# Kernel tuning notes

Measured on AMD Instinct MI355X. Metric: run time of the kernel, lower is better.

## Reference

```python
import jax, jax.numpy as jnp
import numpy as np

CH = 256
DQK = CH // 8


def setup_inputs() -> dict:
    key = jax.random.key(0)
    ks = jax.random.split(key, 8)
    B, C, H, W = 4, CH, 64, 64
    x = jax.random.normal(ks[0], (B, C, H, W), dtype=jnp.float32)
    s = 1.0 / np.sqrt(C)
    Wq = jax.random.normal(ks[1], (DQK, C), dtype=jnp.float32) * s
    bq = jnp.zeros((DQK,), dtype=jnp.float32)
    Wk = jax.random.normal(ks[2], (DQK, C), dtype=jnp.float32) * s
    bk = jnp.zeros((DQK,), dtype=jnp.float32)
    Wv = jax.random.normal(ks[3], (C, C), dtype=jnp.float32) * s
    bv = jnp.zeros((C,), dtype=jnp.float32)
    gamma = jnp.zeros((1,), dtype=jnp.float32)
    return {"x": x, "Wq": Wq, "bq": bq, "Wk": Wk, "bk": bk, "Wv": Wv, "bv": bv, "gamma": gamma}


def reference(x, Wq, bq, Wk, bk, Wv, bv, gamma):
    B, C, H, W = x.shape
    N = H * W
    xf = x.reshape(B, C, N)                                   # [B, C, N]
    # 1x1 convs == per-position linear maps over channels
    q = jnp.einsum('dc,bcn->bdn', Wq, xf) + bq[None, :, None]  # [B, D, N]
    k = jnp.einsum('dc,bcn->bdn', Wk, xf) + bk[None, :, None]  # [B, D, N]
    v = jnp.einsum('oc,bcn->bon', Wv, xf) + bv[None, :, None]  # [B, C, N]
    # energy[b,i,j] = <q[:, i], k[:, j]>  (no 1/sqrt(d) scaling, as in source)
    energy = jnp.einsum('bdi,bdj->bij', q, k)                  # [B, N, N]
    attn = jax.nn.softmax(energy, axis=-1)                     # softmax over j
    # out[b,c,i] = sum_j v[b,c,j] * attn[b,i,j]
    out = jnp.einsum('bcj,bij->bci', v, attn)                  # [B, C, N]
    return x + gamma[0] * out.reshape(B, C, H, W)
```

## Files before the change

### kernel.cpp

```cpp
#include <hip/hip_runtime.h>
#include <hip/hip_bf16.h>

#define NB   4
#define NC   256
#define NPOS 4096
#define NDQK 32

typedef __bf16 bf16x8  __attribute__((ext_vector_type(8)));
typedef float  f32x16  __attribute__((ext_vector_type(16)));

typedef __attribute__((address_space(3))) char*       lds_ptr_t;
typedef const __attribute__((address_space(1))) char* glb_ptr_t;


__global__ __launch_bounds__(256) void proj_kernel(
    const float* __restrict__ x,
    const float* __restrict__ Wq, const float* __restrict__ bq,
    const float* __restrict__ Wk, const float* __restrict__ bk,
    const float* __restrict__ Wv, const float* __restrict__ bv,
    __hip_bfloat16* __restrict__ Qb, __hip_bfloat16* __restrict__ Kb,
    __hip_bfloat16* __restrict__ Vb)
{
    const int t   = threadIdx.x;
    const int l   = t & 63;
    const int w   = t >> 6;
    const int hi  = l >> 5;
    const int col = l & 31;
    const int row = l & 31;

    const int item = blockIdx.x * 4 + w;
    const int th   = item & 1;
    const int nch  = (item >> 1) & 63;
    const int rest = item >> 7;
    const int g    = rest % 5;
    const int b    = rest / 5;

    const float *W0, *W1, *bs0, *bs1;
    int o0 = 0, o1 = 0;
    if (g < 4) {
        o0 = g * 64; o1 = g * 64 + 32;
        W0 = Wv + (size_t)o0 * NC; W1 = Wv + (size_t)o1 * NC;
        bs0 = bv + o0; bs1 = bv + o1;
    } else {
        W0 = Wq; W1 = Wk; bs0 = bq; bs1 = bk;
    }

    bf16x8 wf0[16], wf1[16];
    const float* Wr0 = W0 + (size_t)row * NC + 8 * hi;
    const float* Wr1 = W1 + (size_t)row * NC + 8 * hi;
    #pragma unroll
    for (int kk = 0; kk < 16; ++kk) {
        float4 a0 = *reinterpret_cast<const float4*>(Wr0 + kk * 16);
        float4 c0 = *reinterpret_cast<const float4*>(Wr0 + kk * 16 + 4);
        float4 a1 = *reinterpret_cast<const float4*>(Wr1 + kk * 16);
        float4 c1 = *reinterpret_cast<const float4*>(Wr1 + kk * 16 + 4);
        bf16x8 f0, f1;
        f0[0] = (__bf16)a0.x; f0[1] = (__bf16)a0.y; f0[2] = (__bf16)a0.z; f0[3] = (__bf16)a0.w;
        f0[4] = (__bf16)c0.x; f0[5] = (__bf16)c0.y; f0[6] = (__bf16)c0.z; f0[7] = (__bf16)c0.w;
        f1[0] = (__bf16)a1.x; f1[1] = (__bf16)a1.y; f1[2] = (__bf16)a1.z; f1[3] = (__bf16)a1.w;
        f1[4] = (__bf16)c1.x; f1[5] = (__bf16)c1.y; f1[6] = (__bf16)c1.z; f1[7] = (__bf16)c1.w;
        wf0[kk] = f0; wf1[kk] = f1;
    }

    const int n0 = nch * 64 + th * 32;
    f32x16 acc0, acc1;
    #pragma unroll
    for (int r = 0; r < 16; ++r) { acc0[r] = 0.f; acc1[r] = 0.f; }

    const float* xcol = x + (size_t)b * NC * NPOS + n0 + col;
    #pragma unroll
    for (int kk = 0; kk < 16; ++kk) {
        bf16x8 bf;
        #pragma unroll
        for (int i = 0; i < 8; ++i)
            bf[i] = (__bf16)xcol[(size_t)(kk * 16 + 8 * hi + i) * NPOS];
        acc0 = __builtin_amdgcn_mfma_f32_32x32x16_bf16(wf0[kk], bf, acc0, 0, 0, 0);
        acc1 = __builtin_amdgcn_mfma_f32_32x32x16_bf16(wf1[kk], bf, acc1, 0, 0, 0);
    }

    if (g < 4) {
        __hip_bfloat16* vt = Vb + (size_t)b * NC * NPOS
                                + (size_t)(n0 >> 5) * 8192 + (size_t)g * 2048
                                + ((col >> 4) << 9) + (((col >> 3) & 1) << 8)
                                + (col & 7);
        #pragma unroll
        for (int r = 0; r < 16; ++r) {
            const int orow = (r & 3) + 8 * (r >> 2) + 4 * hi;
            vt[orow * 8]        = __float2bfloat16(acc0[r] + bs0[orow]);
            vt[1024 + orow * 8] = __float2bfloat16(acc1[r] + bs1[orow]);
        }
    } else {
        #pragma unroll
        for (int r = 0; r < 16; ++r) {
            const int orow = (r & 3) + 8 * (r >> 2) + 4 * hi;
            Qb[((size_t)(b * NPOS) + n0 + col) * NDQK + orow] =
                __float2bfloat16((acc0[r] + bs0[orow]) * 1.44269504088896f);
        }
        const int prow = (col & 0x13) | ((col & 4) << 1) | ((col & 8) >> 1);
        __hip_bfloat16* kt = Kb + (size_t)b * (NPOS * 32)
                                + (size_t)(n0 >> 5) * 1024 + prow * 8;
        #pragma unroll
        for (int r = 0; r < 16; ++r) {
            const int orow = (r & 3) + 8 * (r >> 2) + 4 * hi;
            kt[(orow >> 4) * 512 + ((orow >> 3) & 1) * 256 + (orow & 7)] =
                __float2bfloat16(acc1[r] + bs1[orow]);
        }
    }
}

__global__ __launch_bounds__(256, 1) void attn_kernel(
    const __hip_bfloat16* __restrict__ Qb,
    const __hip_bfloat16* __restrict__ Kb,
    const __hip_bfloat16* __restrict__ Vb,
    const float* __restrict__ x,
    const float* __restrict__ gamma,
    float* __restrict__ out)
{
    __shared__ __align__(16) char smem[8192 + 32768 + 16384 + 1024];
    const int t  = threadIdx.x;
    const int l  = t & 63;
    const int w  = t >> 6;
    const int hi = l >> 5;
    const int q  = l & 31;
    const int bx = blockIdx.x;
    const int b  = (bx >> 1) & 3;
    const int qt = ((bx >> 3) << 1) | (bx & 1);
    const int q0 = qt * 64;
    const int c0 = w * 64;

    const __bf16* Qp = reinterpret_cast<const __bf16*>(Qb) + (size_t)b * NPOS * NDQK;
    const __bf16* Kp = reinterpret_cast<const __bf16*>(Kb) + (size_t)b * (NPOS * 32);
    const __bf16* Vp = reinterpret_cast<const __bf16*>(Vb) + (size_t)b * NC * NPOS;

    const bf16x8 qf00 = *reinterpret_cast<const bf16x8*>(Qp + (size_t)(q0 + q) * NDQK + 8 * hi);
    const bf16x8 qf01 = *reinterpret_cast<const bf16x8*>(Qp + (size_t)(q0 + q) * NDQK + 16 + 8 * hi);
    const bf16x8 qf10 = *reinterpret_cast<const bf16x8*>(Qp + (size_t)(q0 + 32 + q) * NDQK + 8 * hi);
    const bf16x8 qf11 = *reinterpret_cast<const bf16x8*>(Qp + (size_t)(q0 + 32 + q) * NDQK + 16 + 8 * hi);
    asm volatile("" :: "v"(qf00), "v"(qf01), "v"(qf10), "v"(qf11));

    char* kb_lds = smem + w * 2048;
    char* vb_lds = smem + 8192 + w * 8192;
    __bf16* kbuf = reinterpret_cast<__bf16*>(kb_lds);
    __bf16* vbuf = reinterpret_cast<__bf16*>(vb_lds);
    __bf16* plds = reinterpret_cast<__bf16*>(smem + 40960);
    float*  lsum = reinterpret_cast<float*>(smem + 57344);

    const __bf16* ksrc = Kp + (size_t)w * 1024 + l * 8;
    const __bf16* vsrc = Vp + (size_t)w * 2048 + l * 8;

    #define DMA16(dst, src) __builtin_amdgcn_global_load_lds( \
        (glb_ptr_t)(const char*)(src), (lds_ptr_t)(dst), 16, 0, 0)
    #define DMAK(tp) do { DMA16(kb_lds, (tp)); DMA16(kb_lds + 1024, (tp) + 512); } while (0)
    #define DMAV(bi, tp) do {                                   \
        DMA16(vb_lds + (bi) * 4096,        (tp));               \
        DMA16(vb_lds + (bi) * 4096 + 1024, (tp) + 512);         \
        DMA16(vb_lds + (bi) * 4096 + 2048, (tp) + 1024);        \
        DMA16(vb_lds + (bi) * 4096 + 3072, (tp) + 1536);        \
    } while (0)

    f32x16 acc00, acc01, acc10, acc11;
    #pragma unroll
    for (int r = 0; r < 16; ++r) { acc00[r] = 0.f; acc01[r] = 0.f; acc10[r] = 0.f; acc11[r] = 0.f; }
    float lp0 = 0.f, lp1 = 0.f;

    f32x16 z16;
    #pragma unroll
    for (int r = 0; r < 16; ++r) z16[r] = 0.f;

    auto PV = [&](int tt, const __bf16* vf) {
        const bf16x8 vc0 = *reinterpret_cast<const bf16x8*>(vf);
        const bf16x8 vc1 = *reinterpret_cast<const bf16x8*>(vf + 512);
        const bf16x8 vc2 = *reinterpret_cast<const bf16x8*>(vf + 1024);
        const bf16x8 vc3 = *reinterpret_cast<const bf16x8*>(vf + 1536);
        const __bf16* pf = plds + tt * 2048 + l * 8;
        const bf16x8 pa00 = *reinterpret_cast<const bf16x8*>(pf);
        const bf16x8 pa01 = *reinterpret_cast<const bf16x8*>(pf + 512);
        const bf16x8 pa10 = *reinterpret_cast<const bf16x8*>(pf + 1024);
        const bf16x8 pa11 = *reinterpret_cast<const bf16x8*>(pf + 1536);
        acc00 = __builtin_amdgcn_mfma_f32_32x32x16_bf16(vc0, pa00, acc00, 0, 0, 0);
        acc00 = __builtin_amdgcn_mfma_f32_32x32x16_bf16(vc1, pa01, acc00, 0, 0, 0);
        acc01 = __builtin_amdgcn_mfma_f32_32x32x16_bf16(vc2, pa00, acc01, 0, 0, 0);
        acc01 = __builtin_amdgcn_mfma_f32_32x32x16_bf16(vc3, pa01, acc01, 0, 0, 0);
        acc10 = __builtin_amdgcn_mfma_f32_32x32x16_bf16(vc0, pa10, acc10, 0, 0, 0);
        acc10 = __builtin_amdgcn_mfma_f32_32x32x16_bf16(vc1, pa11, acc10, 0, 0, 0);
        acc11 = __builtin_amdgcn_mfma_f32_32x32x16_bf16(vc2, pa10, acc11, 0, 0, 0);
        acc11 = __builtin_amdgcn_mfma_f32_32x32x16_bf16(vc3, pa11, acc11, 0, 0, 0);
    };

    DMAK(ksrc);
    DMAV(0, vsrc);

    #pragma unroll 1
    for (int r = 0; r < 32; ++r) {
        asm volatile("s_waitcnt vmcnt(4)" ::: "memory");
        __builtin_amdgcn_sched_barrier(0);
        {
            const bf16x8 kc0 = *reinterpret_cast<const bf16x8*>(kbuf + l * 8);
            const bf16x8 kc1 = *reinterpret_cast<const bf16x8*>(kbuf + 512 + l * 8);
            f32x16 s0 = __builtin_amdgcn_mfma_f32_32x32x16_bf16(kc0, qf00, z16, 0, 0, 0);
            s0 = __builtin_amdgcn_mfma_f32_32x32x16_bf16(kc1, qf01, s0, 0, 0, 0);
            f32x16 s1 = __builtin_amdgcn_mfma_f32_32x32x16_bf16(kc0, qf10, z16, 0, 0, 0);
            s1 = __builtin_amdgcn_mfma_f32_32x32x16_bf16(kc1, qf11, s1, 0, 0, 0);

            float p0[16], p1[16];
            #pragma unroll
            for (int i = 0; i < 16; ++i) p0[i] = __builtin_amdgcn_exp2f(s0[i]);
            #pragma unroll
            for (int i = 0; i < 16; ++i) p1[i] = __builtin_amdgcn_exp2f(s1[i]);

            lp0 += (((p0[0] + p0[1]) + (p0[2] + p0[3])) + ((p0[4] + p0[5]) + (p0[6] + p0[7])))
                 + (((p0[8] + p0[9]) + (p0[10] + p0[11])) + ((p0[12] + p0[13]) + (p0[14] + p0[15])));
            lp1 += (((p1[0] + p1[1]) + (p1[2] + p1[3])) + ((p1[4] + p1[5]) + (p1[6] + p1[7])))
                 + (((p1[8] + p1[9]) + (p1[10] + p1[11])) + ((p1[12] + p1[13]) + (p1[14] + p1[15])));

            bf16x8 pa00, pa01, pa10, pa11;
            #pragma unroll
            for (int i = 0; i < 8; ++i) {
                pa00[i] = (__bf16)p0[i]; pa01[i] = (__bf16)p0[8 + i];
                pa10[i] = (__bf16)p1[i]; pa11[i] = (__bf16)p1[8 + i];
            }
            __bf16* pw = plds + w * 2048 + l * 8;
            *reinterpret_cast<bf16x8*>(pw)        = pa00;
            *reinterpret_cast<bf16x8*>(pw + 512)  = pa01;
            *reinterpret_cast<bf16x8*>(pw + 1024) = pa10;
            *reinterpret_cast<bf16x8*>(pw + 1536) = pa11;
        }
        asm volatile("s_waitcnt lgkmcnt(0)" ::: "memory");
        __builtin_amdgcn_s_barrier();
        __builtin_amdgcn_sched_barrier(0);

        DMAV(1, vsrc + 1 * 8192);
        asm volatile("s_waitcnt vmcnt(4)" ::: "memory");
        __builtin_amdgcn_sched_barrier(0);
        PV(0, vbuf + l * 8);

        asm volatile("s_waitcnt lgkmcnt(0)" ::: "memory");
        __builtin_amdgcn_sched_barrier(0);
        DMAV(0, vsrc + 2 * 8192);
        asm volatile("s_waitcnt vmcnt(4)" ::: "memory");
        __builtin_amdgcn_sched_barrier(0);
        PV(1, vbuf + 2048 + l * 8);

        asm volatile("s_waitcnt lgkmcnt(0)" ::: "memory");
        __builtin_amdgcn_sched_barrier(0);
        DMAV(1, vsrc + 3 * 8192);
        asm volatile("s_waitcnt vmcnt(4)" ::: "memory");
        __builtin_amdgcn_sched_barrier(0);
        PV(2, vbuf + l * 8);

        asm volatile("s_waitcnt lgkmcnt(0)" ::: "memory");
        __builtin_amdgcn_sched_barrier(0);
        ksrc += 4096;
        vsrc += 4 * 8192;
        if (r < 31) {
            DMAK(ksrc);
            DMAV(0, vsrc);
            asm volatile("s_waitcnt vmcnt(6)" ::: "memory");
        } else {
            asm volatile("s_waitcnt vmcnt(0)" ::: "memory");
        }
        __builtin_amdgcn_sched_barrier(0);
        PV(3, vbuf + 2048 + l * 8);

        asm volatile("s_waitcnt lgkmcnt(0)" ::: "memory");
        __builtin_amdgcn_s_barrier();
        __builtin_amdgcn_sched_barrier(0);
    }
    #undef DMA16
    #undef DMAK
    #undef DMAV

    const float lt0 = lp0 + __shfl_xor(lp0, 32);
    const float lt1 = lp1 + __shfl_xor(lp1, 32);
    lsum[w * 64 + 32 * hi + q] = hi ? lt1 : lt0;
    __syncthreads();

    const float gm  = gamma[0];
    const float gl0 = gm / (lsum[q]      + lsum[64 + q]  + lsum[128 + q] + lsum[192 + q]);
    const float gl1 = gm / (lsum[32 + q] + lsum[96 + q]  + lsum[160 + q] + lsum[224 + q]);
    #pragma unroll
    for (int r = 0; r < 16; ++r) {
        const int crow = (r & 3) + 8 * (r >> 2) + 4 * hi;
        const size_t g00 = ((size_t)(b * NC + c0 + crow)) * NPOS + q0 + q;
        const size_t g01 = g00 + (size_t)32 * NPOS;
        out[g00]      = x[g00]      + gl0 * acc00[r];
        out[g01]      = x[g01]      + gl0 * acc01[r];
        out[g00 + 32] = x[g00 + 32] + gl1 * acc10[r];
        out[g01 + 32] = x[g01 + 32] + gl1 * acc11[r];
    }
}

extern "C" void kernel_launch(void* const* d_in, const int* in_sizes, int n_in,
                              void* d_out, int out_size, void* d_ws, size_t ws_size,
                              hipStream_t stream) {
    (void)in_sizes; (void)n_in; (void)out_size; (void)ws_size;
    const float* x     = (const float*)d_in[0];
    const float* Wq    = (const float*)d_in[1];
    const float* bq    = (const float*)d_in[2];
    const float* Wk    = (const float*)d_in[3];
    const float* bk    = (const float*)d_in[4];
    const float* Wv    = (const float*)d_in[5];
    const float* bv    = (const float*)d_in[6];
    const float* gamma = (const float*)d_in[7];
    float* out = (float*)d_out;

    char* ws = (char*)d_ws;
    __hip_bfloat16* Qb = (__hip_bfloat16*)(ws);
    __hip_bfloat16* Kb = (__hip_bfloat16*)(ws + (1u << 20));
    __hip_bfloat16* Vb = (__hip_bfloat16*)(ws + (2u << 20));

    proj_kernel<<<640, 256, 0, stream>>>(x, Wq, bq, Wk, bk, Wv, bv, Qb, Kb, Vb);
    attn_kernel<<<256, 256, 0, stream>>>(Qb, Kb, Vb, x, gamma, out);
}
```

Measured before the change: 91.97 us.

## Deepen V prefetch pipeline to four LDS buffers per wave

Enlarges each wave's V staging area from two to four 4 KB LDS buffers and prefetches a full iteration's worth of V tiles ahead. Each PV step now waits only for its own tile and immediately refills that slot with the next iteration's tile, so global loads overlap more compute. The last iteration is peeled to drain the queue. LDS use grows to about 90 KB per block, which is fine at one block per CU but adds memory pressure and makes the hand-set vmcnt accounting more fragile.

```diff
diff --git a/kernel.cpp b/kernel.cpp
--- a/kernel.cpp
+++ b/kernel.cpp
@@ -116,7 +116,7 @@
     const float* __restrict__ gamma,
     float* __restrict__ out)
 {
-    __shared__ __align__(16) char smem[8192 + 32768 + 16384 + 1024];
+    __shared__ __align__(16) char smem[65536 + 8192 + 16384 + 1024];
     const int t  = threadIdx.x;
     const int l  = t & 63;
     const int w  = t >> 6;
@@ -138,12 +138,12 @@
     const bf16x8 qf11 = *reinterpret_cast<const bf16x8*>(Qp + (size_t)(q0 + 32 + q) * NDQK + 16 + 8 * hi);
     asm volatile("" :: "v"(qf00), "v"(qf01), "v"(qf10), "v"(qf11));
 
-    char* kb_lds = smem + w * 2048;
-    char* vb_lds = smem + 8192 + w * 8192;
-    __bf16* kbuf = reinterpret_cast<__bf16*>(kb_lds);
-    __bf16* vbuf = reinterpret_cast<__bf16*>(vb_lds);
-    __bf16* plds = reinterpret_cast<__bf16*>(smem + 40960);
-    float*  lsum = reinterpret_cast<float*>(smem + 57344);
+    char*   vb_lds = smem + w * 16384;
+    char*   kb_lds = smem + 65536 + w * 2048;
+    __bf16* vbuf   = reinterpret_cast<__bf16*>(vb_lds);
+    __bf16* kbuf   = reinterpret_cast<__bf16*>(kb_lds);
+    __bf16* plds   = reinterpret_cast<__bf16*>(smem + 73728);
+    float*  lsum   = reinterpret_cast<float*>(smem + 90112);
 
     const __bf16* ksrc = Kp + (size_t)w * 1024 + l * 8;
     const __bf16* vsrc = Vp + (size_t)w * 2048 + l * 8;
@@ -151,7 +151,7 @@
     #define DMA16(dst, src) __builtin_amdgcn_global_load_lds( \
         (glb_ptr_t)(const char*)(src), (lds_ptr_t)(dst), 16, 0, 0)
     #define DMAK(tp) do { DMA16(kb_lds, (tp)); DMA16(kb_lds + 1024, (tp) + 512); } while (0)
-    #define DMAV(bi, tp) do {                                   \
+    #define DMAV1(bi, tp) do {                                  \
         DMA16(vb_lds + (bi) * 4096,        (tp));               \
         DMA16(vb_lds + (bi) * 4096 + 1024, (tp) + 512);         \
         DMA16(vb_lds + (bi) * 4096 + 2048, (tp) + 1024);        \
@@ -167,7 +167,40 @@
     #pragma unroll
     for (int r = 0; r < 16; ++r) z16[r] = 0.f;
 
-    auto PV = [&](int tt, const __bf16* vf) {
+    auto QK = [&]() {
+        const bf16x8 kc0 = *reinterpret_cast<const bf16x8*>(kbuf + l * 8);
+        const bf16x8 kc1 = *reinterpret_cast<const bf16x8*>(kbuf + 512 + l * 8);
+        f32x16 s0 = __builtin_amdgcn_mfma_f32_32x32x16_bf16(kc0, qf00, z16, 0, 0, 0);
+        s0 = __builtin_amdgcn_mfma_f32_32x32x16_bf16(kc1, qf01, s0, 0, 0, 0);
+        f32x16 s1 = __builtin_amdgcn_mfma_f32_32x32x16_bf16(kc0, qf10, z16, 0, 0, 0);
+        s1 = __builtin_amdgcn_mfma_f32_32x32x16_bf16(kc1, qf11, s1, 0, 0, 0);
+
+        float p0[16], p1[16];
+        #pragma unroll
+        for (int i = 0; i < 16; ++i) p0[i] = __builtin_amdgcn_exp2f(s0[i]);
+        #pragma unroll
+        for (int i = 0; i < 16; ++i) p1[i] = __builtin_amdgcn_exp2f(s1[i]);
+
+        lp0 += (((p0[0] + p0[1]) + (p0[2] + p0[3])) + ((p0[4] + p0[5]) + (p0[6] + p0[7])))
+             + (((p0[8] + p0[9]) + (p0[10] + p0[11])) + ((p0[12] + p0[13]) + (p0[14] + p0[15])));
+        lp1 += (((p1[0] + p1[1]) + (p1[2] + p1[3])) + ((p1[4] + p1[5]) + (p1[6] + p1[7])))
+             + (((p1[8] + p1[9]) + (p1[10] + p1[11])) + ((p1[12] + p1[13]) + (p1[14] + p1[15])));
+
+        bf16x8 pa00, pa01, pa10, pa11;
+        #pragma unroll
+        for (int i = 0; i < 8; ++i) {
+            pa00[i] = (__bf16)p0[i]; pa01[i] = (__bf16)p0[8 + i];
+            pa10[i] = (__bf16)p1[i]; pa11[i] = (__bf16)p1[8 + i];
+        }
+        __bf16* pw = plds + w * 2048 + l * 8;
+        *reinterpret_cast<bf16x8*>(pw)        = pa00;
+        *reinterpret_cast<bf16x8*>(pw + 512)  = pa01;
+        *reinterpret_cast<bf16x8*>(pw + 1024) = pa10;
+        *reinterpret_cast<bf16x8*>(pw + 1536) = pa11;
+    };
+
+    auto PV = [&](int tt) {
+        const __bf16* vf = vbuf + tt * 2048 + l * 8;
         const bf16x8 vc0 = *reinterpret_cast<const bf16x8*>(vf);
         const bf16x8 vc1 = *reinterpret_cast<const bf16x8*>(vf + 512);
         const bf16x8 vc2 = *reinterpret_cast<const bf16x8*>(vf + 1024);
@@ -187,88 +220,51 @@
         acc11 = __builtin_amdgcn_mfma_f32_32x32x16_bf16(vc3, pa11, acc11, 0, 0, 0);
     };
 
+    #define WAIT(n) do { asm volatile("s_waitcnt vmcnt(" #n ")" ::: "memory"); \
+                         __builtin_amdgcn_sched_barrier(0); } while (0)
+    #define FENCE()  __builtin_amdgcn_sched_barrier(0)
+    #define MIDBAR() do { asm volatile("s_waitcnt lgkmcnt(0)" ::: "memory"); \
+                          __builtin_amdgcn_s_barrier(); FENCE(); } while (0)
+
     DMAK(ksrc);
-    DMAV(0, vsrc);
+    DMAV1(0, vsrc);
+    DMAV1(1, vsrc + 8192);
+    DMAV1(2, vsrc + 2 * 8192);
+    DMAV1(3, vsrc + 3 * 8192);
 
     #pragma unroll 1
-    for (int r = 0; r < 32; ++r) {
-        asm volatile("s_waitcnt vmcnt(4)" ::: "memory");
-        __builtin_amdgcn_sched_barrier(0);
-        {
-            const bf16x8 kc0 = *reinterpret_cast<const bf16x8*>(kbuf + l * 8);
-            const bf16x8 kc1 = *reinterpret_cast<const bf16x8*>(kbuf + 512 + l * 8);
-            f32x16 s0 = __builtin_amdgcn_mfma_f32_32x32x16_bf16(kc0, qf00, z16, 0, 0, 0);
-            s0 = __builtin_amdgcn_mfma_f32_32x32x16_bf16(kc1, qf01, s0, 0, 0, 0);
-            f32x16 s1 = __builtin_amdgcn_mfma_f32_32x32x16_bf16(kc0, qf10, z16, 0, 0, 0);
-            s1 = __builtin_amdgcn_mfma_f32_32x32x16_bf16(kc1, qf11, s1, 0, 0, 0);
-
-            float p0[16], p1[16];
-            #pragma unroll
-            for (int i = 0; i < 16; ++i) p0[i] = __builtin_amdgcn_exp2f(s0[i]);
-            #pragma unroll
-            for (int i = 0; i < 16; ++i) p1[i] = __builtin_amdgcn_exp2f(s1[i]);
-
-            lp0 += (((p0[0] + p0[1]) + (p0[2] + p0[3])) + ((p0[4] + p0[5]) + (p0[6] + p0[7])))
-                 + (((p0[8] + p0[9]) + (p0[10] + p0[11])) + ((p0[12] + p0[13]) + (p0[14] + p0[15])));
-            lp1 += (((p1[0] + p1[1]) + (p1[2] + p1[3])) + ((p1[4] + p1[5]) + (p1[6] + p1[7])))
-                 + (((p1[8] + p1[9]) + (p1[10] + p1[11])) + ((p1[12] + p1[13]) + (p1[14] + p1[15])));
-
-            bf16x8 pa00, pa01, pa10, pa11;
-            #pragma unroll
-            for (int i = 0; i < 8; ++i) {
-                pa00[i] = (__bf16)p0[i]; pa01[i] = (__bf16)p0[8 + i];
-                pa10[i] = (__bf16)p1[i]; pa11[i] = (__bf16)p1[8 + i];
-            }
-            __bf16* pw = plds + w * 2048 + l * 8;
-            *reinterpret_cast<bf16x8*>(pw)        = pa00;
-            *reinterpret_cast<bf16x8*>(pw + 512)  = pa01;
-            *reinterpret_cast<bf16x8*>(pw + 1024) = pa10;
-            *reinterpret_cast<bf16x8*>(pw + 1536) = pa11;
-        }
-        asm volatile("s_waitcnt lgkmcnt(0)" ::: "memory");
-        __builtin_amdgcn_s_barrier();
-        __builtin_amdgcn_sched_barrier(0);
-
-        DMAV(1, vsrc + 1 * 8192);
-        asm volatile("s_waitcnt vmcnt(4)" ::: "memory");
-        __builtin_amdgcn_sched_barrier(0);
-        PV(0, vbuf + l * 8);
-
-        asm volatile("s_waitcnt lgkmcnt(0)" ::: "memory");
-        __builtin_amdgcn_sched_barrier(0);
-        DMAV(0, vsrc + 2 * 8192);
-        asm volatile("s_waitcnt vmcnt(4)" ::: "memory");
-        __builtin_amdgcn_sched_barrier(0);
-        PV(1, vbuf + 2048 + l * 8);
-
-        asm volatile("s_waitcnt lgkmcnt(0)" ::: "memory");
-        __builtin_amdgcn_sched_barrier(0);
-        DMAV(1, vsrc + 3 * 8192);
-        asm volatile("s_waitcnt vmcnt(4)" ::: "memory");
-        __builtin_amdgcn_sched_barrier(0);
-        PV(2, vbuf + l * 8);
-
-        asm volatile("s_waitcnt lgkmcnt(0)" ::: "memory");
-        __builtin_amdgcn_sched_barrier(0);
+    for (int r = 0; r < 31; ++r) {
+        WAIT(16);
+        QK();
+        MIDBAR();
+
         ksrc += 4096;
-        vsrc += 4 * 8192;
-        if (r < 31) {
-            DMAK(ksrc);
-            DMAV(0, vsrc);
-            asm volatile("s_waitcnt vmcnt(6)" ::: "memory");
-        } else {
-            asm volatile("s_waitcnt vmcnt(0)" ::: "memory");
-        }
-        __builtin_amdgcn_sched_barrier(0);
-        PV(3, vbuf + 2048 + l * 8);
-
-        asm volatile("s_waitcnt lgkmcnt(0)" ::: "memory");
-        __builtin_amdgcn_s_barrier();
-        __builtin_amdgcn_sched_barrier(0);
-    }
+        DMAK(ksrc);
+        FENCE();
+
+        const __bf16* vnext = vsrc + 4 * 8192;
+        WAIT(14);  PV(0);  FENCE();  DMAV1(0, vnext);             FENCE();
+        WAIT(14);  PV(1);  FENCE();  DMAV1(1, vnext + 8192);      FENCE();
+        WAIT(14);  PV(2);  FENCE();  DMAV1(2, vnext + 2 * 8192);  FENCE();
+        WAIT(14);  PV(3);  FENCE();  DMAV1(3, vnext + 3 * 8192);  FENCE();
+        vsrc = vnext;
+
+        MIDBAR();
+    }
+    WAIT(16);
+    QK();
+    MIDBAR();
+    WAIT(12);  PV(0);
+    WAIT(8);   PV(1);
+    WAIT(4);   PV(2);
+    WAIT(0);   PV(3);
+
     #undef DMA16
     #undef DMAK
-    #undef DMAV
+    #undef DMAV1
+    #undef WAIT
+    #undef FENCE
+    #undef MIDBAR
 
     const float lt0 = lp0 + __shfl_xor(lp0, 32);
     const float lt1 = lp1 + __shfl_xor(lp1, 32);
```

After: 87.09 us. 5.3% less time.
